# Performance work log

Measured on AMD Instinct MI355X. Metric: run time of the kernel, lower is better.

The kernel has to match this reference:

```python
import jax, jax.numpy as jnp
import numpy as np

NUM_FIELDS = 32
EMBED = 64
ATTN = 64
BATCH = 2048

# all field pairs (i < j), NC2 = 496
_ROW, _COL = np.triu_indices(NUM_FIELDS, k=1)
ROW_IDX = jnp.asarray(_ROW, dtype=jnp.int32)
COL_IDX = jnp.asarray(_COL, dtype=jnp.int32)


def setup_inputs() -> dict:
    key = jax.random.key(0)
    k0, k1, k2 = jax.random.split(key, 3)
    inputs = jax.random.normal(k0, (BATCH, NUM_FIELDS, EMBED), dtype=jnp.float32)
    # Linear init ~ U(-1/sqrt(fan_in), 1/sqrt(fan_in)) style scale
    W1 = jax.random.normal(k1, (EMBED, ATTN), dtype=jnp.float32) / jnp.sqrt(float(EMBED))
    b1 = jnp.zeros((ATTN,), dtype=jnp.float32)
    w2 = jax.random.normal(k2, (ATTN, 1), dtype=jnp.float32) / jnp.sqrt(float(ATTN))
    b2 = jnp.zeros((1,), dtype=jnp.float32)
    return {"inputs": inputs, "W1": W1, "b1": b1, "w2": w2, "b2": b2}


def reference(inputs, W1, b1, w2, b2):
    # inner: (B, P, E) pairwise elementwise products of field embeddings
    inner = inputs[:, ROW_IDX, :] * inputs[:, COL_IDX, :]
    # tiny 2-layer MLP attention: (B, P, E) -> (B, P, A) -> (B, P, 1)
    h = jax.nn.relu(jnp.einsum('bpe,ea->bpa', inner, W1) + b1)
    logits = jnp.einsum('bpa,ao->bpo', h, w2) + b2          # (B, P, 1)
    attn_scores = jax.nn.softmax(logits, axis=1)            # softmax over pair dim
    # softmax-weighted sum over pairs -> (B, E), then (B, 1, E)
    outputs = jnp.sum(attn_scores * inner, axis=1)
    return outputs[:, None, :], attn_scores
```

## Files before the change

kernel.cpp:

```cpp
#include <hip/hip_runtime.h>
#include <math.h>

#define NF 32
#define NE 64
#define NA 64
#define NP 496

typedef __attribute__((ext_vector_type(8))) _Float16 f16x8;
typedef __attribute__((ext_vector_type(4))) _Float16 f16x4;
typedef __attribute__((ext_vector_type(2))) __fp16   h16x2;
typedef __attribute__((ext_vector_type(4))) float    f32x4;

#define W1T_S 72
#define XT_S  40
#define WT_S  40

__global__ __launch_bounds__(256, 1) void afm_fwd(
    const float* __restrict__ x,
    const float* __restrict__ W1,
    const float* __restrict__ b1,
    const float* __restrict__ w2,
    const float* __restrict__ b2,
    float* __restrict__ out,
    float* __restrict__ attn,
    int B)
{
    const int tid   = threadIdx.x;
    const int lane  = tid & 63;
    const int wv    = tid >> 6;
    const int smp   = wv >> 1;
    const int sub   = wv & 1;
    const int nlane = lane & 15;
    const int g     = lane >> 4;

    __shared__ __align__(16) _Float16 W1t[64][W1T_S];
    __shared__ __align__(16) _Float16 xh[2][8][NF][8];
    __shared__ __align__(16) _Float16 xT[2][NE][XT_S];
    __shared__ __align__(16) _Float16 Wt[2][NF][WT_S];
    __shared__ float s_l[2][NP];
    __shared__ unsigned short s_rc[512];

    {
        const int e = tid & 63, a0 = (tid >> 6) << 4;
        const float* wr = W1 + e * NA + a0;
        #pragma unroll
        for (int i = 0; i < 4; ++i) {
            const float4 v = *(const float4*)(wr + 4 * i);
            W1t[a0 + 4*i + 0][e] = (_Float16)v.x;
            W1t[a0 + 4*i + 1][e] = (_Float16)v.y;
            W1t[a0 + 4*i + 2][e] = (_Float16)v.z;
            W1t[a0 + 4*i + 3][e] = (_Float16)v.w;
        }
    }
    for (int p = tid; p < 512; p += 256) {
        const int pp = (p < NP) ? p : NP - 1;
        const float sq = sqrtf((float)(3969 - 8 * pp));
        int r = (int)((63.0f - sq) * 0.5f);
        int st = (r * (63 - r)) >> 1;
        if (pp < st) { --r; st = (r * (63 - r)) >> 1; }
        else { const int st2 = ((r + 1) * (62 - r)) >> 1; if (pp >= st2) { ++r; st = st2; } }
        const int c = pp - st + r + 1;
        s_rc[p] = (unsigned short)(r | (c << 8));
    }

    int b = blockIdx.x * 2 + smp;
    if (b >= B) b = B - 1;

    {
        unsigned int* wz = (unsigned int*)&Wt[smp][0][0];
        #pragma unroll
        for (int i = 0; i < 5; ++i) {
            const int idx = i * 64 + lane;
            if (idx < 320) wz[sub * 320 + idx] = 0u;
        }
    }

    const float* __restrict__ xb = x + (size_t)b * (NF * NE);
    {
        const int r  = sub * 16 + (lane >> 2);
        const int e0 = (lane & 3) << 4;
        #pragma unroll
        for (int i = 0; i < 4; ++i) {
            const int e = e0 + 4 * i;
            const float4 v = *(const float4*)(xb + r * NE + e);
            f16x4 hv = { (_Float16)v.x, (_Float16)v.y, (_Float16)v.z, (_Float16)v.w };
            *(f16x4*)&xh[smp][e >> 3][r][e & 7] = hv;
            xT[smp][e + 0][r] = hv[0];
            xT[smp][e + 1][r] = hv[1];
            xT[smp][e + 2][r] = hv[2];
            xT[smp][e + 3][r] = hv[3];
        }
    }

    int pr, pc;
    {
        const int p0 = 31 * nlane + 16 * sub;
        const float sq = sqrtf((float)(3969 - 8 * p0));
        int r = (int)((63.0f - sq) * 0.5f);
        int st = (r * (63 - r)) >> 1;
        if (p0 < st) { --r; st = (r * (63 - r)) >> 1; }
        else { const int st2 = ((r + 1) * (62 - r)) >> 1; if (p0 >= st2) { ++r; st = st2; } }
        pr = r;
        pc = p0 - st + r + 1;
    }
    __syncthreads();

    f16x8 w1f[2][4];
    #pragma unroll
    for (int s = 0; s < 2; ++s)
        #pragma unroll
        for (int mt = 0; mt < 4; ++mt)
            w1f[s][mt] = *(const f16x8*)&W1t[mt * 16 + nlane][s * 32 + g * 8];

    f32x4 b1q[4];
    h16x2 w2h[4][2];
    #pragma unroll
    for (int mt = 0; mt < 4; ++mt) {
        b1q[mt] = *(const f32x4*)(b1 + mt * 16 + g * 4);
        const f32x4 wq = *(const f32x4*)(w2 + mt * 16 + g * 4);
        w2h[mt][0] = (h16x2){ (__fp16)wq[0], (__fp16)wq[1] };
        w2h[mt][1] = (h16x2){ (__fp16)wq[2], (__fp16)wq[3] };
    }
    const float bias2 = b2[0];
    const h16x2 zz = { (__fp16)0.0f, (__fp16)0.0f };

    #pragma unroll
    for (int t = 0; t < 16; ++t) {
        if (16 * sub + t < 31) {
            f16x8 af[2];
            #pragma unroll
            for (int s = 0; s < 2; ++s) {
                const f16x8 xr8 = *(const f16x8*)&xh[smp][4 * s + g][pr][0];
                const f16x8 xc8 = *(const f16x8*)&xh[smp][4 * s + g][pc][0];
                af[s] = xr8 * xc8;
            }
            f32x4 acc[4];
            __builtin_amdgcn_s_setprio(1);
            #pragma unroll
            for (int mt = 0; mt < 4; ++mt)
                acc[mt] = __builtin_amdgcn_mfma_f32_16x16x32_f16(w1f[0][mt], af[0], b1q[mt], 0, 0, 0);
            #pragma unroll
            for (int mt = 0; mt < 4; ++mt)
                acc[mt] = __builtin_amdgcn_mfma_f32_16x16x32_f16(w1f[1][mt], af[1], acc[mt], 0, 0, 0);
            __builtin_amdgcn_s_setprio(0);

            float plA = 0.f, plB = 0.f;
            #pragma unroll
            for (int mt = 0; mt < 4; ++mt) {
                h16x2 h01 = __builtin_amdgcn_cvt_pkrtz(acc[mt][0], acc[mt][1]);
                h16x2 h23 = __builtin_amdgcn_cvt_pkrtz(acc[mt][2], acc[mt][3]);
                h01 = __builtin_elementwise_max(h01, zz);
                h23 = __builtin_elementwise_max(h23, zz);
                plA = __builtin_amdgcn_fdot2(h01, w2h[mt][0], plA, false);
                plB = __builtin_amdgcn_fdot2(h23, w2h[mt][1], plB, false);
            }
            float logit = plA + plB;
            logit += __shfl_xor(logit, 16);
            logit += __shfl_xor(logit, 32);
            if (lane < 16) s_l[smp][31 * lane + 16 * sub + t] = logit + bias2;

            ++pc;
            const int wrap = (pc >= 32) ? 1 : 0;
            pr += wrap;
            pc = wrap ? (pr + 1) : pc;
        }
    }
    __syncthreads();

    float lv[8], mx = -1e30f;
    #pragma unroll
    for (int k = 0; k < 8; ++k) {
        const int p = (k << 6) + lane;
        lv[k] = (p < NP) ? s_l[smp][p] : -1e30f;
        mx = fmaxf(mx, lv[k]);
    }
    #pragma unroll
    for (int off = 1; off < 64; off <<= 1) mx = fmaxf(mx, __shfl_xor(mx, off));

    float ev[8], se = 0.0f;
    #pragma unroll
    for (int k = 0; k < 8; ++k) {
        const int p = (k << 6) + lane;
        ev[k] = (p < NP) ? __expf(lv[k] - mx) : 0.0f;
        se += ev[k];
    }
    #pragma unroll
    for (int off = 1; off < 64; off <<= 1) se += __shfl_xor(se, off);
    const float inv = 1.0f / se;

    float* __restrict__ attn_b = attn + (size_t)b * NP;
    #pragma unroll
    for (int k = 0; k < 4; ++k) {
        const int kk = (sub << 2) + k;
        const int p = (kk << 6) + lane;
        if (p < NP) {
            const float w = ev[kk] * inv;
            attn_b[p] = w;
            const unsigned short rc = s_rc[p];
            const int r = rc & 255, c = rc >> 8;
            const _Float16 wh = (_Float16)w;
            Wt[smp][r][c] = wh;
            Wt[smp][c][r] = wh;
        }
    }
    __syncthreads();

    f16x8 wa[2], xbf[2];
    #pragma unroll
    for (int mt = 0; mt < 2; ++mt)
        wa[mt] = *(const f16x8*)&Wt[smp][mt * 16 + nlane][g * 8];
    #pragma unroll
    for (int j = 0; j < 2; ++j) {
        const int nt = 2 * sub + j;
        xbf[j] = *(const f16x8*)&xT[smp][nt * 16 + nlane][g * 8];
    }

    f32x4 y[2][2];
    #pragma unroll
    for (int mt = 0; mt < 2; ++mt)
        #pragma unroll
        for (int j = 0; j < 2; ++j) {
            y[mt][j] = (f32x4)0.0f;
            y[mt][j] = __builtin_amdgcn_mfma_f32_16x16x32_f16(wa[mt], xbf[j], y[mt][j], 0, 0, 0);
        }

    float po[2] = {0.f, 0.f};
    #pragma unroll
    for (int j = 0; j < 2; ++j) {
        const int nt = 2 * sub + j;
        #pragma unroll
        for (int mt = 0; mt < 2; ++mt) {
            const f16x4 xv = *(const f16x4*)&xT[smp][nt * 16 + nlane][mt * 16 + g * 4];
            po[j] += (float)xv[0] * y[mt][j][0];
            po[j] += (float)xv[1] * y[mt][j][1];
            po[j] += (float)xv[2] * y[mt][j][2];
            po[j] += (float)xv[3] * y[mt][j][3];
        }
        po[j] += __shfl_xor(po[j], 16);
        po[j] += __shfl_xor(po[j], 32);
    }
    if (lane < 16) {
        float* __restrict__ ob = out + (size_t)b * NE;
        #pragma unroll
        for (int j = 0; j < 2; ++j)
            ob[(2 * sub + j) * 16 + lane] = 0.5f * po[j];
    }
}

extern "C" void kernel_launch(void* const* d_in, const int* in_sizes, int n_in,
                              void* d_out, int out_size, void* d_ws, size_t ws_size,
                              hipStream_t stream) {
    const float* x  = (const float*)d_in[0];
    const float* W1 = (const float*)d_in[1];
    const float* b1 = (const float*)d_in[2];
    const float* w2 = (const float*)d_in[3];
    const float* b2 = (const float*)d_in[4];

    const int B = in_sizes[0] / (NF * NE);
    float* out_p  = (float*)d_out;
    float* attn_p = (float*)d_out + (size_t)B * NE;

    afm_fwd<<<(B + 1) / 2, 256, 0, stream>>>(x, W1, b1, w2, b2, out_p, attn_p, B);
}
```

Before: 24.49 us.

## Remap pair tiling to fixed column per lane with prefetched row loads

Replaces the sequential pair walk (sqrt-based start index plus per-step row/column wrap) with a mapping where each of the 16 lanes owns two fixed partner columns (j+1 and the complementary 31-j). The column embeddings are loaded into registers once and reused across all 16 steps, and the next row is software-prefetched from shared memory each iteration. The remapping also lets both sub-waves process 16 evenly balanced steps with no guard branch. Launch bounds now request 4 blocks per CU, which caps register use and may cause spills given the extra held fragments.

```diff
diff --git a/kernel.cpp b/kernel.cpp
--- a/kernel.cpp
+++ b/kernel.cpp
@@ -15,7 +15,7 @@
 #define XT_S  40
 #define WT_S  40
 
-__global__ __launch_bounds__(256, 1) void afm_fwd(
+__global__ __launch_bounds__(256, 4) void afm_fwd(
     const float* __restrict__ x,
     const float* __restrict__ W1,
     const float* __restrict__ b1,
@@ -91,18 +91,6 @@
             xT[smp][e + 3][r] = hv[3];
         }
     }
-
-    int pr, pc;
-    {
-        const int p0 = 31 * nlane + 16 * sub;
-        const float sq = sqrtf((float)(3969 - 8 * p0));
-        int r = (int)((63.0f - sq) * 0.5f);
-        int st = (r * (63 - r)) >> 1;
-        if (p0 < st) { --r; st = (r * (63 - r)) >> 1; }
-        else { const int st2 = ((r + 1) * (62 - r)) >> 1; if (p0 >= st2) { ++r; st = st2; } }
-        pr = r;
-        pc = p0 - st + r + 1;
-    }
     __syncthreads();
 
     f16x8 w1f[2][4];
@@ -124,46 +112,67 @@
     const float bias2 = b2[0];
     const h16x2 zz = { (__fp16)0.0f, (__fp16)0.0f };
 
+    const int c1 = nlane + 1;
+    const int c2 = (nlane < 15) ? (31 - nlane) : 16;
+
+    const f16x8 xc1h0 = *(const f16x8*)&xh[smp][g][c1][0];
+    const f16x8 xc1h1 = *(const f16x8*)&xh[smp][4 + g][c1][0];
+    const f16x8 xc2h0 = *(const f16x8*)&xh[smp][g][c2][0];
+    const f16x8 xc2h1 = *(const f16x8*)&xh[smp][4 + g][c2][0];
+
+    int s0 = 16 * sub;
+    int r_cur = (s0 >= c1) ? (s0 - c1) : s0;
+    f16x8 xr_h0 = *(const f16x8*)&xh[smp][g][r_cur][0];
+    f16x8 xr_h1 = *(const f16x8*)&xh[smp][4 + g][r_cur][0];
+
     #pragma unroll
     for (int t = 0; t < 16; ++t) {
-        if (16 * sub + t < 31) {
-            f16x8 af[2];
-            #pragma unroll
-            for (int s = 0; s < 2; ++s) {
-                const f16x8 xr8 = *(const f16x8*)&xh[smp][4 * s + g][pr][0];
-                const f16x8 xc8 = *(const f16x8*)&xh[smp][4 * s + g][pc][0];
-                af[s] = xr8 * xc8;
-            }
-            f32x4 acc[4];
-            __builtin_amdgcn_s_setprio(1);
-            #pragma unroll
-            for (int mt = 0; mt < 4; ++mt)
-                acc[mt] = __builtin_amdgcn_mfma_f32_16x16x32_f16(w1f[0][mt], af[0], b1q[mt], 0, 0, 0);
-            #pragma unroll
-            for (int mt = 0; mt < 4; ++mt)
-                acc[mt] = __builtin_amdgcn_mfma_f32_16x16x32_f16(w1f[1][mt], af[1], acc[mt], 0, 0, 0);
-            __builtin_amdgcn_s_setprio(0);
-
-            float plA = 0.f, plB = 0.f;
-            #pragma unroll
-            for (int mt = 0; mt < 4; ++mt) {
-                h16x2 h01 = __builtin_amdgcn_cvt_pkrtz(acc[mt][0], acc[mt][1]);
-                h16x2 h23 = __builtin_amdgcn_cvt_pkrtz(acc[mt][2], acc[mt][3]);
-                h01 = __builtin_elementwise_max(h01, zz);
-                h23 = __builtin_elementwise_max(h23, zz);
-                plA = __builtin_amdgcn_fdot2(h01, w2h[mt][0], plA, false);
-                plB = __builtin_amdgcn_fdot2(h23, w2h[mt][1], plB, false);
-            }
-            float logit = plA + plB;
-            logit += __shfl_xor(logit, 16);
-            logit += __shfl_xor(logit, 32);
-            if (lane < 16) s_l[smp][31 * lane + 16 * sub + t] = logit + bias2;
-
-            ++pc;
-            const int wrap = (pc >= 32) ? 1 : 0;
-            pr += wrap;
-            pc = wrap ? (pr + 1) : pc;
-        }
+        const int s = 16 * sub + t;
+        const bool second = (s >= c1);
+        const int r = second ? (s - c1) : s;
+        const int c = second ? c2 : c1;
+
+        f16x8 xrn_h0, xrn_h1;
+        if (t < 15) {
+            const int sn = s + 1;
+            const int rn = (sn >= c1) ? (sn - c1) : sn;
+            xrn_h0 = *(const f16x8*)&xh[smp][g][rn][0];
+            xrn_h1 = *(const f16x8*)&xh[smp][4 + g][rn][0];
+        }
+
+        const f16x8 xch0 = second ? xc2h0 : xc1h0;
+        const f16x8 xch1 = second ? xc2h1 : xc1h1;
+        const f16x8 af0 = xr_h0 * xch0;
+        const f16x8 af1 = xr_h1 * xch1;
+
+        f32x4 acc[4];
+        __builtin_amdgcn_s_setprio(1);
+        #pragma unroll
+        for (int mt = 0; mt < 4; ++mt)
+            acc[mt] = __builtin_amdgcn_mfma_f32_16x16x32_f16(w1f[0][mt], af0, b1q[mt], 0, 0, 0);
+        #pragma unroll
+        for (int mt = 0; mt < 4; ++mt)
+            acc[mt] = __builtin_amdgcn_mfma_f32_16x16x32_f16(w1f[1][mt], af1, acc[mt], 0, 0, 0);
+        __builtin_amdgcn_s_setprio(0);
+
+        float plA = 0.f, plB = 0.f;
+        #pragma unroll
+        for (int mt = 0; mt < 4; ++mt) {
+            h16x2 h01 = __builtin_amdgcn_cvt_pkrtz(acc[mt][0], acc[mt][1]);
+            h16x2 h23 = __builtin_amdgcn_cvt_pkrtz(acc[mt][2], acc[mt][3]);
+            h01 = __builtin_elementwise_max(h01, zz);
+            h23 = __builtin_elementwise_max(h23, zz);
+            plA = __builtin_amdgcn_fdot2(h01, w2h[mt][0], plA, false);
+            plB = __builtin_amdgcn_fdot2(h23, w2h[mt][1], plB, false);
+        }
+        float logit = plA + plB;
+        logit += __shfl_xor(logit, 16);
+        logit += __shfl_xor(logit, 32);
+
+        const int p = ((r * (63 - r)) >> 1) + c - r - 1;
+        if (lane < 16) s_l[smp][p] = logit + bias2;
+
+        xr_h0 = xrn_h0; xr_h1 = xrn_h1;
     }
     __syncthreads();
 
```

Measured after the change: 24.12 us. No clear change (-1.5%).
